# Kernel tuning notes

Measured on AMD Instinct MI355X. Metric: run time of the kernel, lower is better.

## Reference

```python
import jax, jax.numpy as jnp
import numpy as np

NUM_HEADS = 4
NUM_GROUPS = 8
EPS = 1e-5


def group_norm(x, w, b):
    # x: [B, C, H, W], 8 groups, per-channel affine
    B, C, H, W = x.shape
    g = x.reshape(B, NUM_GROUPS, C // NUM_GROUPS, H, W)
    mu = g.mean(axis=(2, 3, 4), keepdims=True)
    var = g.var(axis=(2, 3, 4), keepdims=True)
    g = (g - mu) * jax.lax.rsqrt(var + EPS)
    x = g.reshape(B, C, H, W)
    return x * w[None, :, None, None] + b[None, :, None, None]


def setup_inputs() -> dict:
    key = jax.random.key(0)
    ks = jax.random.split(key, 7)
    B, C, H, W = 16, 256, 32, 32
    x = jax.random.normal(ks[0], (B, C, H, W), dtype=jnp.float32)
    norm_w = jnp.ones((C,), jnp.float32)
    norm_b = jnp.zeros((C,), jnp.float32)
    # 1x1 convs == channel matmuls; fan-in scaled init
    qkv_w = jax.random.normal(ks[1], (3 * C, C), dtype=jnp.float32) / np.sqrt(C)
    qkv_b = jnp.zeros((3 * C,), jnp.float32)
    proj_w = jax.random.normal(ks[2], (C, C), dtype=jnp.float32) / np.sqrt(C)
    proj_b = jnp.zeros((C,), jnp.float32)
    return {"x": x, "norm_w": norm_w, "norm_b": norm_b,
            "qkv_w": qkv_w, "qkv_b": qkv_b,
            "proj_w": proj_w, "proj_b": proj_b}


def reference(x, norm_w, norm_b, qkv_w, qkv_b, proj_w, proj_b):
    B, C, H, W = x.shape
    nh = NUM_HEADS
    d = C // nh
    N = H * W

    h = group_norm(x, norm_w, norm_b)
    # 1x1 conv -> channel matmul: [B, 3C, H, W]
    qkv = jnp.einsum('oc,bchw->bohw', qkv_w, h) + qkv_b[None, :, None, None]
    qkv = qkv.reshape(B, 3, nh, d, N)
    q, k, v = qkv[:, 0], qkv[:, 1], qkv[:, 2]  # [B, nh, d, N]

    scale = d ** (-0.5)
    attn = jnp.einsum('bhcn,bhcm->bhnm', q, k) * scale  # [B, nh, N, N]
    attn = jax.nn.softmax(attn, axis=-1)
    out = jnp.einsum('bhnm,bhcm->bhcn', attn, v)  # [B, nh, d, N]
    out = out.reshape(B, C, H, W)
    out = jnp.einsum('oc,bchw->bohw', proj_w, out) + proj_b[None, :, None, None]
    return x + out
```

## Files before the change

### kernel.cpp

```cpp
#include <hip/hip_runtime.h>
#include <math.h>

#define BATCH 16
#define CH 256
#define NG 8
#define NH 4
#define HD 64
#define NN 1024
#define GSZ 32
#define GELEMS (GSZ * NN)

typedef __attribute__((ext_vector_type(8))) __bf16 bf16x8;
typedef __attribute__((ext_vector_type(4))) __bf16 bf16x4;
typedef __attribute__((ext_vector_type(4))) _Float16 f16x4;
typedef __attribute__((ext_vector_type(4))) float f32x4;

__device__ __forceinline__ unsigned short f2b(float f) {
    union { __bf16 h; unsigned short u; } c; c.h = (__bf16)f; return c.u;
}
__device__ __forceinline__ unsigned short f2h(float f) {
    union { _Float16 h; unsigned short u; } c; c.h = (_Float16)f; return c.u;
}

#define MFMA(a, b, c) __builtin_amdgcn_mfma_f32_16x16x32_bf16(a, b, c, 0, 0, 0)
#define MFMA16(a, b, c) __builtin_amdgcn_mfma_f32_16x16x16f16(a, b, c, 0, 0, 0)

__global__ __launch_bounds__(256) void prep_kernel(
    const float* __restrict__ x, const float* __restrict__ qkv_w,
    const float* __restrict__ proj_w, float* __restrict__ stats,
    unsigned short* __restrict__ wq, unsigned short* __restrict__ wp)
{
    int tid = threadIdx.x;
    if (blockIdx.x >= 128) {
        int t = (blockIdx.x - 128) * 256 + tid;
        const float* src; unsigned short* dst; size_t off;
        if (t < 24576) { src = qkv_w; dst = wq; off = (size_t)t * 8; }
        else           { src = proj_w; dst = wp; off = (size_t)(t - 24576) * 8; }
        const float4* s4 = (const float4*)(src + off);
        float4 a = s4[0], b = s4[1];
        bf16x8 pk;
        pk[0] = (__bf16)a.x; pk[1] = (__bf16)a.y; pk[2] = (__bf16)a.z; pk[3] = (__bf16)a.w;
        pk[4] = (__bf16)b.x; pk[5] = (__bf16)b.y; pk[6] = (__bf16)b.z; pk[7] = (__bf16)b.w;
        *(bf16x8*)(dst + off) = pk;
        return;
    }
    int b = blockIdx.x >> 3, g = blockIdx.x & 7;
    const float4* x4 = (const float4*)(x + ((size_t)b * CH + g * GSZ) * NN);
    float s = 0.f, ss = 0.f;
    #pragma unroll
    for (int i = 0; i < 32; ++i) {
        float4 v = x4[tid + i * 256];
        s  += v.x + v.y + v.z + v.w;
        ss += v.x * v.x + v.y * v.y + v.z * v.z + v.w * v.w;
    }
    #pragma unroll
    for (int off = 1; off < 64; off <<= 1) {
        s  += __shfl_xor(s, off);
        ss += __shfl_xor(ss, off);
    }
    __shared__ float red[8];
    int wave = tid >> 6, lane = tid & 63;
    if (lane == 0) { red[wave] = s; red[4 + wave] = ss; }
    __syncthreads();
    if (tid == 0) {
        float ts  = red[0] + red[1] + red[2] + red[3];
        float tss = red[4] + red[5] + red[6] + red[7];
        float mu  = ts * (1.f / GELEMS);
        float var = tss * (1.f / GELEMS) - mu * mu;
        stats[blockIdx.x * 2] = mu;
        stats[blockIdx.x * 2 + 1] = rsqrtf(var + 1e-5f);
    }
}

__global__ __launch_bounds__(256) void gn_apply_kernel(
    const float* __restrict__ x, const float* __restrict__ w,
    const float* __restrict__ bb, const float* __restrict__ stats,
    unsigned short* __restrict__ hT)
{
    __shared__ float Ts[64][68];
    __shared__ float wcp[256], bcp[256];
    const int b = blockIdx.y, n0 = blockIdx.x * 64;
    const int tid = threadIdx.x;
    {
        int c = tid, g = c >> 5;
        float mu = stats[(b * 8 + g) * 2], rs = stats[(b * 8 + g) * 2 + 1];
        float wc = w[c] * rs;
        wcp[c] = wc; bcp[c] = bb[c] - mu * wc;
    }
    __syncthreads();
    const float* xb = x + (size_t)b * CH * NN;
    const int c_l = tid >> 2, nq = tid & 3;
    const int n_l = tid >> 2, cq = tid & 3;
    for (int cb = 0; cb < 4; ++cb) {
        #pragma unroll
        for (int i = 0; i < 4; ++i)
            *(float4*)&Ts[c_l][nq * 4 + i * 16] =
                *(const float4*)(xb + (size_t)(cb * 64 + c_l) * NN + n0 + nq * 4 + i * 16);
        __syncthreads();
        #pragma unroll
        for (int s = 0; s < 2; ++s) {
            int cbase = cq * 16 + s * 8;
            bf16x8 pk;
            #pragma unroll
            for (int j = 0; j < 8; ++j) {
                int c = cb * 64 + cbase + j;
                pk[j] = (__bf16)(Ts[cbase + j][n_l] * wcp[c] + bcp[c]);
            }
            *(bf16x8*)(hT + ((size_t)b * NN + n0 + n_l) * CH + cb * 64 + cbase) = pk;
        }
        __syncthreads();
    }
}

template <int KIND>
__global__ __launch_bounds__(256) void gemm_kernel(
    const unsigned short* __restrict__ AT,
    const unsigned short* __restrict__ Wb,
    const float* __restrict__ bias,
    unsigned short* __restrict__ outT, unsigned short* __restrict__ outV,
    const float* __restrict__ res, float* __restrict__ out)
{
    __shared__ __align__(16) unsigned short Ws[64][136];
    __shared__ __align__(16) unsigned short Hs[64][136];
    const int b = blockIdx.z, o0 = blockIdx.y * 64, n0 = blockIdx.x * 64;
    const int tid = threadIdx.x;
    const int lane = tid & 63, wv = tid >> 6;
    const int l = lane & 15, quad = lane >> 4;
    const int iw = wv & 1, jw = wv >> 1;
    const bool qk_mode = (KIND == 0) && (blockIdx.y < 8);
    const int r4 = tid >> 2, c4 = tid & 3;

    f32x4 acc[2][2] = {};
    for (int st = 0; st < 2; ++st) {
        const int cc0 = st * 128;
        #pragma unroll
        for (int i = 0; i < 4; ++i) {
            int ch = c4 + i * 4;
            *(bf16x8*)&Ws[r4][ch * 8] =
                *(const bf16x8*)(Wb + (size_t)(o0 + r4) * CH + cc0 + ch * 8);
            *(bf16x8*)&Hs[r4][ch * 8] =
                *(const bf16x8*)(AT + ((size_t)b * NN + n0 + r4) * CH + cc0 + ch * 8);
        }
        __syncthreads();
        #pragma unroll
        for (int kt = 0; kt < 4; ++kt) {
            bf16x8 af[2], bf[2];
            #pragma unroll
            for (int i = 0; i < 2; ++i)
                af[i] = *(const bf16x8*)&Hs[iw * 32 + i * 16 + l][kt * 32 + quad * 8];
            #pragma unroll
            for (int j = 0; j < 2; ++j)
                bf[j] = *(const bf16x8*)&Ws[jw * 32 + j * 16 + l][kt * 32 + quad * 8];
            #pragma unroll
            for (int i = 0; i < 2; ++i)
                #pragma unroll
                for (int j = 0; j < 2; ++j)
                    acc[i][j] = qk_mode ? MFMA(af[i], bf[j], acc[i][j])
                                        : MFMA(bf[j], af[i], acc[i][j]);
        }
        __syncthreads();
    }

    #pragma unroll
    for (int i = 0; i < 2; ++i)
        #pragma unroll
        for (int j = 0; j < 2; ++j) {
            if (qk_mode) {
                int o = o0 + jw * 32 + j * 16 + l;
                float bs = bias[o];
                #pragma unroll
                for (int r = 0; r < 4; ++r) {
                    int n = n0 + iw * 32 + i * 16 + quad * 4 + r;
                    outT[((size_t)b * NN + n) * 512 + o] = f2b(acc[i][j][r] + bs);
                }
            } else {
                int o = o0 + jw * 32 + j * 16 + quad * 4;
                int n = n0 + iw * 32 + i * 16 + l;
                #pragma unroll
                for (int r = 0; r < 4; ++r) {
                    float v = acc[i][j][r] + bias[o + r];
                    if (KIND == 0)
                        outV[((size_t)b * CH + (o + r - 512)) * NN + n] = f2h(v);
                    else {
                        size_t idx = ((size_t)b * CH + o + r) * NN + n;
                        out[idx] = v + res[idx];
                    }
                }
            }
        }
}

__global__ __launch_bounds__(256, 3) void attn_kernel(
    const unsigned short* __restrict__ qkvT,
    const unsigned short* __restrict__ vbuf,
    unsigned short* __restrict__ ctxT)
{
    __shared__ __align__(16) unsigned short KV[2][8192];
    __shared__ float Lred[2][32];
    const int id = blockIdx.x;
    const int bh = id & 63, nt = id >> 6;
    const int b = bh >> 2, hh = bh & 3;
    const int n0 = nt * 64;
    const int tid = threadIdx.x;
    const int lane = tid & 63, w = tid >> 6;
    const int l = lane & 15, quad = lane >> 4;
    const int qx = w & 1, ky = w >> 1;
    const float KL2E = 0.125f * 1.44269504f;
    const int r4 = tid >> 2, c4 = tid & 3;

    bf16x8 qf[2][2];
    {
        const unsigned short* qp = qkvT + ((size_t)b * NN + n0 + 32 * qx + l) * 512 + hh * 64;
        #pragma unroll
        for (int ns = 0; ns < 2; ++ns)
            #pragma unroll
            for (int kt = 0; kt < 2; ++kt)
                qf[ns][kt] = *(const bf16x8*)(qp + (size_t)ns * 16 * 512 + kt * 32 + quad * 8);
    }

    const unsigned short* gk = qkvT + ((size_t)b * NN + r4) * 512 + 256 + hh * 64;
    const unsigned short* gv = vbuf + ((size_t)b * CH + hh * 64 + r4) * NN;
    const int p0 = (c4 ^ (r4 & 7)) * 8, p1 = ((c4 + 4) ^ (r4 & 7)) * 8;

    bf16x8 kpre0, kpre1, vpre0, vpre1;
    kpre0 = *(const bf16x8*)(gk + c4 * 8);
    kpre1 = *(const bf16x8*)(gk + (c4 + 4) * 8);
    vpre0 = *(const bf16x8*)(gv + c4 * 8);
    vpre1 = *(const bf16x8*)(gv + (c4 + 4) * 8);
    *(bf16x8*)&KV[0][r4 * 64 + p0] = kpre0;
    *(bf16x8*)&KV[0][r4 * 64 + p1] = kpre1;
    *(bf16x8*)&KV[0][4096 + r4 * 64 + p0] = vpre0;
    *(bf16x8*)&KV[0][4096 + r4 * 64 + p1] = vpre1;
    __syncthreads();

    float l_w[2] = {0.f, 0.f};
    f32x4 oacc[2][4] = {};

    for (int mt = 0; mt < 16; ++mt) {
        const int cur = mt & 1;
        if (mt < 15) {
            const unsigned short* gk1 = gk + (size_t)(mt + 1) * 64 * 512;
            const unsigned short* gv1 = gv + (mt + 1) * 64;
            kpre0 = *(const bf16x8*)(gk1 + c4 * 8);
            kpre1 = *(const bf16x8*)(gk1 + (c4 + 4) * 8);
            vpre0 = *(const bf16x8*)(gv1 + c4 * 8);
            vpre1 = *(const bf16x8*)(gv1 + (c4 + 4) * 8);
        }

        bf16x8 kf[2][2];
        #pragma unroll
        for (int mt2 = 0; mt2 < 2; ++mt2)
            #pragma unroll
            for (int kt = 0; kt < 2; ++kt)
                kf[mt2][kt] = *(const bf16x8*)
                    &KV[cur][(32 * ky + 16 * mt2 + l) * 64 + (((kt * 4 + quad) ^ (l & 7)) * 8)];

        f32x4 sacc[2][2] = {};
        #pragma unroll
        for (int kt = 0; kt < 2; ++kt)
            #pragma unroll
            for (int mt2 = 0; mt2 < 2; ++mt2)
                #pragma unroll
                for (int ns = 0; ns < 2; ++ns)
                    sacc[mt2][ns] = MFMA(kf[mt2][kt], qf[ns][kt], sacc[mt2][ns]);

        f16x4 pf[2][2];
        #pragma unroll
        for (int mt2 = 0; mt2 < 2; ++mt2)
            #pragma unroll
            for (int ns = 0; ns < 2; ++ns)
                #pragma unroll
                for (int r = 0; r < 4; ++r) {
                    float p = exp2f(sacc[mt2][ns][r] * KL2E);
                    l_w[ns] += p;
                    pf[mt2][ns][r] = (_Float16)p;
                }

        #pragma unroll
        for (int mt2 = 0; mt2 < 2; ++mt2) {
            const int q8 = 4 * ky + 2 * mt2 + (quad >> 1);
            const int vo = ((q8 ^ (l & 7)) * 8) + (quad & 1) * 4;
            #pragma unroll
            for (int ct = 0; ct < 4; ++ct) {
                f16x4 va = *(const f16x4*)&KV[cur][4096 + (16 * ct + l) * 64 + vo];
                #pragma unroll
                for (int ns = 0; ns < 2; ++ns)
                    oacc[ns][ct] = MFMA16(va, pf[mt2][ns], oacc[ns][ct]);
            }
        }

        if (mt < 15) {
            const int nxt = cur ^ 1;
            *(bf16x8*)&KV[nxt][r4 * 64 + p0] = kpre0;
            *(bf16x8*)&KV[nxt][r4 * 64 + p1] = kpre1;
            *(bf16x8*)&KV[nxt][4096 + r4 * 64 + p0] = vpre0;
            *(bf16x8*)&KV[nxt][4096 + r4 * 64 + p1] = vpre1;
            __syncthreads();
        }
    }

    #pragma unroll
    for (int ns = 0; ns < 2; ++ns) {
        l_w[ns] += __shfl_xor(l_w[ns], 16);
        l_w[ns] += __shfl_xor(l_w[ns], 32);
    }
    float* Ored = (float*)&KV[0][0];
    if (ky == 1) {
        #pragma unroll
        for (int ns = 0; ns < 2; ++ns) {
            if (quad == 0) Lred[qx][ns * 16 + l] = l_w[ns];
            #pragma unroll
            for (int ct = 0; ct < 4; ++ct)
                #pragma unroll
                for (int r = 0; r < 4; ++r)
                    Ored[qx * 2048 + (16 * ct + quad * 4 + r) * 32 + ns * 16 + l] =
                        oacc[ns][ct][r];
        }
    }
    __syncthreads();
    if (ky == 0) {
        unsigned short* cb = ctxT + ((size_t)b * NN + n0 + 32 * qx) * CH + hh * 64;
        #pragma unroll
        for (int ns = 0; ns < 2; ++ns) {
            float inv = 1.f / (l_w[ns] + Lred[qx][ns * 16 + l]);
            #pragma unroll
            for (int ct = 0; ct < 4; ++ct) {
                bf16x4 pk;
                #pragma unroll
                for (int r = 0; r < 4; ++r)
                    pk[r] = (__bf16)((oacc[ns][ct][r] +
                             Ored[qx * 2048 + (16 * ct + quad * 4 + r) * 32 + ns * 16 + l]) * inv);
                *(bf16x4*)(cb + (size_t)(ns * 16 + l) * CH + 16 * ct + quad * 4) = pk;
            }
        }
    }
}

extern "C" void kernel_launch(void* const* d_in, const int* in_sizes, int n_in,
                              void* d_out, int out_size, void* d_ws, size_t ws_size,
                              hipStream_t stream)
{
    const float* x      = (const float*)d_in[0];
    const float* norm_w = (const float*)d_in[1];
    const float* norm_b = (const float*)d_in[2];
    const float* qkv_w  = (const float*)d_in[3];
    const float* qkv_b  = (const float*)d_in[4];
    const float* proj_w = (const float*)d_in[5];
    const float* proj_b = (const float*)d_in[6];
    float* out = (float*)d_out;

    unsigned short* hT   = (unsigned short*)d_ws;
    unsigned short* qkvT = hT   + (size_t)BATCH * NN * CH;
    unsigned short* vbuf = qkvT + (size_t)BATCH * NN * 512;
    unsigned short* ctxT = vbuf + (size_t)BATCH * CH * NN;
    unsigned short* wq   = ctxT + (size_t)BATCH * NN * CH;
    unsigned short* wp   = wq + (size_t)768 * CH;
    float* stats         = (float*)(wp + (size_t)CH * CH);

    prep_kernel<<<dim3(256), 256, 0, stream>>>(x, qkv_w, proj_w, stats, wq, wp);
    gn_apply_kernel<<<dim3(16, BATCH), 256, 0, stream>>>(x, norm_w, norm_b, stats, hT);
    gemm_kernel<0><<<dim3(NN / 64, 12, BATCH), 256, 0, stream>>>(
        hT, wq, qkv_b, qkvT, vbuf, nullptr, nullptr);
    attn_kernel<<<dim3(1024), 256, 0, stream>>>(qkvT, vbuf, ctxT);
    gemm_kernel<1><<<dim3(NN / 64, 4, BATCH), 256, 0, stream>>>(
        ctxT, wp, proj_b, nullptr, nullptr, x, out);
}
```

Baseline: 147.9 us.

## Enlarge GEMM tiles to 128x128 with XOR-swizzled shared memory

Both channel-matmul GEMM kernels now use 128x128 output tiles and step the K dimension in 64-wide chunks, so each wave computes a 4x4 grid of MFMA tiles instead of 2x2. More MFMA work is done per shared-memory load, which raises data reuse. The padded LDS rows are replaced with an XOR swizzle to avoid bank conflicts. In exchange, each wave holds more accumulator registers and the grids have fewer blocks (768 and 256), which may reduce occupancy or leave compute units idle. The GEMMs are only part of the total time, which is dominated by attention.

```diff
diff --git a/kernel.cpp b/kernel.cpp
--- a/kernel.cpp
+++ b/kernel.cpp
@@ -120,62 +120,64 @@
     unsigned short* __restrict__ outT, unsigned short* __restrict__ outV,
     const float* __restrict__ res, float* __restrict__ out)
 {
-    __shared__ __align__(16) unsigned short Ws[64][136];
-    __shared__ __align__(16) unsigned short Hs[64][136];
-    const int b = blockIdx.z, o0 = blockIdx.y * 64, n0 = blockIdx.x * 64;
+    __shared__ __align__(16) unsigned short Hs[128 * 64];
+    __shared__ __align__(16) unsigned short Wl[128 * 64];
+    const int b = blockIdx.z, o0 = blockIdx.y * 128, n0 = blockIdx.x * 128;
     const int tid = threadIdx.x;
-    const int lane = tid & 63, wv = tid >> 6;
+    const int lane = tid & 63, w = tid >> 6;
     const int l = lane & 15, quad = lane >> 4;
-    const int iw = wv & 1, jw = wv >> 1;
-    const bool qk_mode = (KIND == 0) && (blockIdx.y < 8);
-    const int r4 = tid >> 2, c4 = tid & 3;
-
-    f32x4 acc[2][2] = {};
-    for (int st = 0; st < 2; ++st) {
-        const int cc0 = st * 128;
+    const int iw = w & 1, jw = w >> 1;
+    const bool qk_mode = (KIND == 0) && (blockIdx.y < 4);
+    const int sr = tid >> 3, sc = tid & 7;
+
+    f32x4 acc[4][4] = {};
+    for (int cc = 0; cc < 4; ++cc) {
+        const int cc0 = cc * 64;
         #pragma unroll
         for (int i = 0; i < 4; ++i) {
-            int ch = c4 + i * 4;
-            *(bf16x8*)&Ws[r4][ch * 8] =
-                *(const bf16x8*)(Wb + (size_t)(o0 + r4) * CH + cc0 + ch * 8);
-            *(bf16x8*)&Hs[r4][ch * 8] =
-                *(const bf16x8*)(AT + ((size_t)b * NN + n0 + r4) * CH + cc0 + ch * 8);
+            int r = sr + i * 32;
+            int p = (sc ^ (r & 7)) * 8;
+            *(bf16x8*)&Hs[r * 64 + p] =
+                *(const bf16x8*)(AT + ((size_t)b * NN + n0 + r) * CH + cc0 + sc * 8);
+            *(bf16x8*)&Wl[r * 64 + p] =
+                *(const bf16x8*)(Wb + (size_t)(o0 + r) * CH + cc0 + sc * 8);
         }
         __syncthreads();
         #pragma unroll
-        for (int kt = 0; kt < 4; ++kt) {
-            bf16x8 af[2], bf[2];
-            #pragma unroll
-            for (int i = 0; i < 2; ++i)
-                af[i] = *(const bf16x8*)&Hs[iw * 32 + i * 16 + l][kt * 32 + quad * 8];
-            #pragma unroll
-            for (int j = 0; j < 2; ++j)
-                bf[j] = *(const bf16x8*)&Ws[jw * 32 + j * 16 + l][kt * 32 + quad * 8];
-            #pragma unroll
-            for (int i = 0; i < 2; ++i)
-                #pragma unroll
-                for (int j = 0; j < 2; ++j)
-                    acc[i][j] = qk_mode ? MFMA(af[i], bf[j], acc[i][j])
-                                        : MFMA(bf[j], af[i], acc[i][j]);
+        for (int kt = 0; kt < 2; ++kt) {
+            const int q = ((kt * 4 + quad) ^ (l & 7)) * 8;
+            bf16x8 hf[4], wf[4];
+            #pragma unroll
+            for (int i = 0; i < 4; ++i)
+                hf[i] = *(const bf16x8*)&Hs[(iw * 64 + i * 16 + l) * 64 + q];
+            #pragma unroll
+            for (int j = 0; j < 4; ++j)
+                wf[j] = *(const bf16x8*)&Wl[(jw * 64 + j * 16 + l) * 64 + q];
+            #pragma unroll
+            for (int i = 0; i < 4; ++i)
+                #pragma unroll
+                for (int j = 0; j < 4; ++j)
+                    acc[i][j] = qk_mode ? MFMA(hf[i], wf[j], acc[i][j])
+                                        : MFMA(wf[j], hf[i], acc[i][j]);
         }
         __syncthreads();
     }
 
     #pragma unroll
-    for (int i = 0; i < 2; ++i)
-        #pragma unroll
-        for (int j = 0; j < 2; ++j) {
+    for (int i = 0; i < 4; ++i)
+        #pragma unroll
+        for (int j = 0; j < 4; ++j) {
             if (qk_mode) {
-                int o = o0 + jw * 32 + j * 16 + l;
+                int o = o0 + jw * 64 + j * 16 + l;
                 float bs = bias[o];
                 #pragma unroll
                 for (int r = 0; r < 4; ++r) {
-                    int n = n0 + iw * 32 + i * 16 + quad * 4 + r;
+                    int n = n0 + iw * 64 + i * 16 + quad * 4 + r;
                     outT[((size_t)b * NN + n) * 512 + o] = f2b(acc[i][j][r] + bs);
                 }
             } else {
-                int o = o0 + jw * 32 + j * 16 + quad * 4;
-                int n = n0 + iw * 32 + i * 16 + l;
+                int o = o0 + jw * 64 + j * 16 + quad * 4;
+                int n = n0 + iw * 64 + i * 16 + l;
                 #pragma unroll
                 for (int r = 0; r < 4; ++r) {
                     float v = acc[i][j][r] + bias[o + r];
@@ -359,9 +361,9 @@
 
     prep_kernel<<<dim3(256), 256, 0, stream>>>(x, qkv_w, proj_w, stats, wq, wp);
     gn_apply_kernel<<<dim3(16, BATCH), 256, 0, stream>>>(x, norm_w, norm_b, stats, hT);
-    gemm_kernel<0><<<dim3(NN / 64, 12, BATCH), 256, 0, stream>>>(
+    gemm_kernel<0><<<dim3(8, 6, BATCH), 256, 0, stream>>>(
         hT, wq, qkv_b, qkvT, vbuf, nullptr, nullptr);
     attn_kernel<<<dim3(1024), 256, 0, stream>>>(qkvT, vbuf, ctxT);
-    gemm_kernel<1><<<dim3(NN / 64, 4, BATCH), 256, 0, stream>>>(
+    gemm_kernel<1><<<dim3(8, 2, BATCH), 256, 0, stream>>>(
         ctxT, wp, proj_b, nullptr, nullptr, x, out);
 }
```

Result: slower. 166.0 us (+12.2%).
